# Kernel tuning notes

Measured on AMD Instinct MI355X. Metric: run time of the kernel, lower is better.

## Reference

```python
import jax, jax.numpy as jnp
import numpy as np

N = 50000      # nodes
E = 800000     # edges (avg degree 16)
F_IN = 128     # input_dim
HID = 64       # hidden_dim
HEADS = 4      # heads on first layer only
G = 512        # number of graphs in batch
EPS = 1e-5
NEG_SLOPE = 0.2

# (in_dim, out_dim, heads) per GATv2 layer
LAYER_DIMS = [(F_IN, HID, HEADS), (HID * HEADS, HID, 1), (HID, HID, 1)]


def setup_inputs() -> dict:
    key = jax.random.key(0)
    ks = jax.random.split(key, 16)
    def rn(k, shape, fan_in):
        return jax.random.normal(k, shape, jnp.float32) / np.float32(np.sqrt(fan_in))
    inp = {}
    inp["x"] = jax.random.normal(ks[0], (N, F_IN), jnp.float32)
    inp["edge_index"] = jax.random.randint(ks[1], (2, E), 0, N)
    inp["batch"] = jnp.sort(jax.random.randint(ks[2], (N,), 0, G))
    i = 3
    for l, (din, dout, h) in enumerate(LAYER_DIMS):
        kk = jax.random.split(ks[i], 3)
        inp[f"Wl{l}"] = rn(kk[0], (din, h * dout), din)
        inp[f"bl{l}"] = jnp.zeros((h * dout,), jnp.float32)
        inp[f"Wr{l}"] = rn(kk[1], (din, h * dout), din)
        inp[f"br{l}"] = jnp.zeros((h * dout,), jnp.float32)
        inp[f"att{l}"] = rn(kk[2], (h, dout), dout)
        inp[f"bias{l}"] = jnp.zeros((h * dout,), jnp.float32)
        inp[f"ln_g{l}"] = jnp.ones((h * dout,), jnp.float32)
        inp[f"ln_b{l}"] = jnp.zeros((h * dout,), jnp.float32)
        i += 1
    inp["Wh1"] = rn(ks[i], (HID, HID), HID)
    inp["bh1"] = jnp.zeros((HID,), jnp.float32)
    inp["Wh2"] = rn(ks[i + 1], (HID, 1), HID)
    inp["bh2"] = jnp.zeros((1,), jnp.float32)
    return inp


def gatv2_layer(x, src, dst, Wl, bl, Wr, br, att, bias, heads, out_c):
    """PyG GATv2Conv (concat=True, share_weights=False, eval mode)."""
    n = x.shape[0]
    xl = (x @ Wl + bl).reshape(n, heads, out_c)   # messages (source side)
    xr = (x @ Wr + br).reshape(n, heads, out_c)   # destination side
    e = jax.nn.leaky_relu(xl[src] + xr[dst], NEG_SLOPE)          # [E,H,C]
    logit = jnp.einsum('ehc,hc->eh', e, att)                      # [E,H]
    m = jax.ops.segment_max(logit, dst, num_segments=n)           # segment-softmax
    ex = jnp.exp(logit - m[dst])
    den = jax.ops.segment_sum(ex, dst, num_segments=n)
    alpha = ex / den[dst]                                         # [E,H]
    out = jax.ops.segment_sum(alpha[:, :, None] * xl[src], dst, num_segments=n)
    return out.reshape(n, heads * out_c) + bias


def graph_layernorm(h, g, b):
    """PyG LayerNorm(mode='graph') with batch=None: normalize over all elements."""
    mu = h.mean()
    xc = h - mu
    var = (xc * xc).mean()
    return xc * jax.lax.rsqrt(var + EPS) * g + b


def reference(x, edge_index, batch,
              Wl0, bl0, Wr0, br0, att0, bias0, ln_g0, ln_b0,
              Wl1, bl1, Wr1, br1, att1, bias1, ln_g1, ln_b1,
              Wl2, bl2, Wr2, br2, att2, bias2, ln_g2, ln_b2,
              Wh1, bh1, Wh2, bh2):
    src, dst = edge_index[0], edge_index[1]
    layers = [
        (Wl0, bl0, Wr0, br0, att0, bias0, ln_g0, ln_b0),
        (Wl1, bl1, Wr1, br1, att1, bias1, ln_g1, ln_b1),
        (Wl2, bl2, Wr2, br2, att2, bias2, ln_g2, ln_b2),
    ]
    h = x
    for (Wl, bl, Wr, br, att, bias, g, b), (_, dout, heads) in zip(layers, LAYER_DIMS):
        h_in = h
        h = gatv2_layer(h, src, dst, Wl, bl, Wr, br, att, bias, heads, dout)
        h = graph_layernorm(h, g, b)
        h = jax.nn.relu(h)
        if h_in.shape[1] == h.shape[1]:   # residual only when widths match
            h = h + h_in
        # dropout: identity in eval mode
    # global mean pool over graphs
    counts = jax.ops.segment_sum(jnp.ones((h.shape[0], 1), h.dtype), batch, num_segments=G)
    Z = jax.ops.segment_sum(h, batch, num_segments=G) / jnp.maximum(counts, 1.0)
    logits = jax.nn.relu(Z @ Wh1 + bh1) @ Wh2 + bh2
    return logits
```

## Files before the change

### kernel.cpp

```cpp
#include <hip/hip_runtime.h>
#include <math.h>

#define NN 50000
#define NE 800000
#define NG 512
#define LRELU 0.2f
#define LN_EPS 1e-5
#define GCAP 128
#define NBUCK 256

typedef __attribute__((ext_vector_type(8))) short short8;
typedef __attribute__((ext_vector_type(4))) float f32x4;

__global__ void hist_kernel(const int* __restrict__ dst, int* __restrict__ deg) {
    int e = blockIdx.x * blockDim.x + threadIdx.x;
    if (e < NE) atomicAdd(&deg[dst[e]], 1);
}

__global__ __launch_bounds__(1024) void scan1(const int* __restrict__ deg,
                                              int* __restrict__ excl,
                                              int* __restrict__ bsum, int n) {
    __shared__ int s[1024];
    int tid = threadIdx.x;
    int gid = blockIdx.x * 1024 + tid;
    int v = (gid < n) ? deg[gid] : 0;
    s[tid] = v;
    __syncthreads();
    for (int off = 1; off < 1024; off <<= 1) {
        int t = (tid >= off) ? s[tid - off] : 0;
        __syncthreads();
        s[tid] += t;
        __syncthreads();
    }
    if (gid < n) excl[gid] = s[tid] - v;
    if (tid == 1023) bsum[blockIdx.x] = s[1023];
}

__global__ __launch_bounds__(1024) void scan3(int* __restrict__ row_ptr,
                                              int* __restrict__ cursor,
                                              const int* __restrict__ bsum, int n) {
    __shared__ int sbase;
    int tid = threadIdx.x;
    if (tid < 64) {
        int v = (tid < (int)blockIdx.x) ? bsum[tid] : 0;
        #pragma unroll
        for (int off = 32; off > 0; off >>= 1) v += __shfl_xor(v, off, 64);
        if (tid == 0) sbase = v;
    }
    __syncthreads();
    int gid = blockIdx.x * 1024 + tid;
    if (gid < n) {
        int v = row_ptr[gid] + sbase;
        row_ptr[gid] = v;
        cursor[gid] = v;
    }
    if (gid == 0) row_ptr[n] = NE;
}

__global__ void scatter_kernel(const int* __restrict__ src, const int* __restrict__ dst,
                               int* __restrict__ cursor, int* __restrict__ col_src) {
    int e = blockIdx.x * blockDim.x + threadIdx.x;
    if (e < NE) {
        int pos = atomicAdd(&cursor[dst[e]], 1);
        col_src[pos] = src[e];
    }
}

__device__ inline void split_bf16(float v, ushort& h, ushort& l) {
    unsigned ub = __float_as_uint(v);
    unsigned hh = (ub + 0x7FFFu + ((ub >> 16) & 1u)) >> 16;
    float vh = __uint_as_float(hh << 16);
    float r = v - vh;
    unsigned ur = __float_as_uint(r);
    unsigned ll = (ur + 0x7FFFu + ((ur >> 16) & 1u)) >> 16;
    h = (ushort)hh; l = (ushort)ll;
}

__global__ __launch_bounds__(256) void prep_w(const float* __restrict__ Wl0,
                                              const float* __restrict__ Wr0,
                                              const float* __restrict__ Wl1,
                                              const float* __restrict__ Wr1,
                                              const float* __restrict__ Wl2,
                                              const float* __restrict__ Wr2,
                                              ushort* __restrict__ wt) {
    int id = blockIdx.x * 256 + threadIdx.x;
    const float* W; int K, N, rel; ushort* hi;
    if (id < 65536) {
        W = (id < 32768) ? Wl0 : Wr0;
        rel = id & 32767; K = 128; N = 256;
        hi = wt + ((id < 32768) ? 0 : 65536);
    } else if (id < 98304) {
        int t = id - 65536;
        W = (t < 16384) ? Wl1 : Wr1;
        rel = t & 16383; K = 256; N = 64;
        hi = wt + 131072 + ((t < 16384) ? 0 : 32768);
    } else if (id < 106496) {
        int t = id - 98304;
        W = (t < 4096) ? Wl2 : Wr2;
        rel = t & 4095; K = 64; N = 64;
        hi = wt + 196608 + ((t < 4096) ? 0 : 8192);
    } else return;
    ushort* lo = hi + K * N;
    int n = rel / K, k = rel - n * K;
    ushort h, l;
    split_bf16(W[k * N + n], h, l);
    hi[rel] = h;
    lo[rel] = l;
}

template<int NCB, bool DUAL, bool DOLN>
__global__ __launch_bounds__(256) void gemm_mfma(const float* __restrict__ A,
                                                 const ushort* __restrict__ Bh0,
                                                 const ushort* __restrict__ Bl0,
                                                 const float* __restrict__ bias0,
                                                 float* __restrict__ C0,
                                                 const ushort* __restrict__ Bh1,
                                                 const ushort* __restrict__ Bl1,
                                                 const float* __restrict__ bias1,
                                                 float* __restrict__ C1,
                                                 int M, int Ncol, int K,
                                                 const double* __restrict__ red,
                                                 int Mdiv,
                                                 const float* __restrict__ lng,
                                                 const float* __restrict__ lnb) {
    __shared__ ushort sAh[64][40];
    __shared__ ushort sAl[64][40];
    __shared__ ushort sBh[64 * NCB][40];
    __shared__ ushort sBl[64 * NCB][40];
    __shared__ float sstat[2];
    const ushort* Bhi = (!DUAL && blockIdx.y) ? Bh1 : Bh0;
    const ushort* Blo = (!DUAL && blockIdx.y) ? Bl1 : Bl0;
    const float*  biasS = (!DUAL && blockIdx.y) ? bias1 : bias0;
    float*        CS = (!DUAL && blockIdx.y) ? C1 : C0;
    const int tid = threadIdx.x;
    const int row0 = blockIdx.x * 64;
    const int w = tid >> 6, lane = tid & 63;
    const int fm = lane & 15;
    const int fk = (lane >> 4) * 8;
    float mu = 0.f, rstd = 0.f;
    if constexpr (DOLN) {
        if (tid < 64) {
            double sa = 0, sb = 0;
            for (int i = lane; i < NBUCK; i += 64) { sa += red[2 * i]; sb += red[2 * i + 1]; }
            #pragma unroll
            for (int off = 32; off > 0; off >>= 1) {
                sa += __shfl_xor(sa, off, 64);
                sb += __shfl_xor(sb, off, 64);
            }
            if (lane == 0) {
                double m_ = sa / Mdiv;
                double v_ = sb / Mdiv - m_ * m_;
                sstat[0] = (float)m_;
                sstat[1] = (float)(1.0 / sqrt(v_ + LN_EPS));
            }
        }
        __syncthreads();
        mu = sstat[0]; rstd = sstat[1];
    }
    f32x4 acc[4 * NCB] = {};

    for (int k0 = 0; k0 < K; k0 += 32) {
        __syncthreads();
        int f = tid;
        #pragma unroll
        for (int it = 0; it < 2; it++, f += 256) {
            int r = f >> 3, kc = (f & 7) * 4;
            int grow = row0 + r;
            float4 v = (grow < M) ? *(const float4*)&A[(size_t)grow * K + k0 + kc]
                                  : make_float4(0.f, 0.f, 0.f, 0.f);
            if constexpr (DOLN) {
                int c0 = k0 + kc;
                v.x = fmaxf((v.x - mu) * rstd * lng[c0 + 0] + lnb[c0 + 0], 0.f);
                v.y = fmaxf((v.y - mu) * rstd * lng[c0 + 1] + lnb[c0 + 1], 0.f);
                v.z = fmaxf((v.z - mu) * rstd * lng[c0 + 2] + lnb[c0 + 2], 0.f);
                v.w = fmaxf((v.w - mu) * rstd * lng[c0 + 3] + lnb[c0 + 3], 0.f);
            }
            ushort4 h, l;
            split_bf16(v.x, h.x, l.x);
            split_bf16(v.y, h.y, l.y);
            split_bf16(v.z, h.z, l.z);
            split_bf16(v.w, h.w, l.w);
            *(ushort4*)&sAh[r][kc] = h;
            *(ushort4*)&sAl[r][kc] = l;
        }
        int u = tid;
        #pragma unroll
        for (int it = 0; it < 2 * NCB; it++, u += 256) {
            int n = u >> 3, kc = (u & 7) * 4;
            const ushort* ph; const ushort* pl; int nr;
            if constexpr (DUAL) {
                bool s1 = n >= (32 * NCB);
                ph = s1 ? Bh1 : Bh0; pl = s1 ? Bl1 : Bl0;
                nr = s1 ? n - 32 * NCB : n;
            } else {
                ph = Bhi; pl = Blo; nr = n;
            }
            *(ushort4*)&sBh[n][kc] = *(const ushort4*)&ph[(size_t)nr * K + k0 + kc];
            *(ushort4*)&sBl[n][kc] = *(const ushort4*)&pl[(size_t)nr * K + k0 + kc];
        }
        __syncthreads();
        short8 ah = *(const short8*)&sAh[w * 16 + fm][fk];
        short8 al = *(const short8*)&sAl[w * 16 + fm][fk];
        #pragma unroll
        for (int c = 0; c < 4 * NCB; c++) {
            short8 bh = *(const short8*)&sBh[c * 16 + fm][fk];
            short8 bl = *(const short8*)&sBl[c * 16 + fm][fk];
            acc[c] = __builtin_amdgcn_mfma_f32_16x16x32_bf16(ah, bh, acc[c], 0, 0, 0);
            acc[c] = __builtin_amdgcn_mfma_f32_16x16x32_bf16(al, bh, acc[c], 0, 0, 0);
            acc[c] = __builtin_amdgcn_mfma_f32_16x16x32_bf16(ah, bl, acc[c], 0, 0, 0);
        }
    }
    const int orow = w * 16 + (lane >> 4) * 4;
    #pragma unroll
    for (int c = 0; c < 4 * NCB; c++) {
        float* Cp; const float* bp; int col;
        if constexpr (DUAL) {
            bool s1 = c >= 2 * NCB;
            Cp = s1 ? C1 : C0; bp = s1 ? bias1 : bias0;
            col = (s1 ? c - 2 * NCB : c) * 16 + fm;
        } else {
            Cp = CS; bp = biasS;
            col = c * 16 + fm;
        }
        float bv = bp[col];
        #pragma unroll
        for (int r = 0; r < 4; r++) {
            int grow = row0 + orow + r;
            if (grow < M) Cp[(size_t)grow * Ncol + col] = acc[c][r] + bv;
        }
    }
}

__device__ inline float dpp_red_add16(float x) {
    x += __int_as_float(__builtin_amdgcn_update_dpp(0, __float_as_int(x), 0xB1, 0xF, 0xF, true));
    x += __int_as_float(__builtin_amdgcn_update_dpp(0, __float_as_int(x), 0x4E, 0xF, 0xF, true));
    x += __int_as_float(__builtin_amdgcn_update_dpp(0, __float_as_int(x), 0x141, 0xF, 0xF, true));
    x += __int_as_float(__builtin_amdgcn_update_dpp(0, __float_as_int(x), 0x140, 0xF, 0xF, true));
    return x;
}

__device__ inline void gat_upd_fast(const float4& xv, const float4& rxr, const float4& ratt,
                                    float& m, float& sum, float4& acc) {
    float vx = xv.x + rxr.x; vx = fmaxf(vx, vx * LRELU);
    float vy = xv.y + rxr.y; vy = fmaxf(vy, vy * LRELU);
    float vz = xv.z + rxr.z; vz = fmaxf(vz, vz * LRELU);
    float vw = xv.w + rxr.w; vw = fmaxf(vw, vw * LRELU);
    float p = vx * ratt.x;
    p = fmaf(vy, ratt.y, p);
    p = fmaf(vz, ratt.z, p);
    p = fmaf(vw, ratt.w, p);
    p = dpp_red_add16(p);
    if (__all(p <= m)) {
        float e = __expf(p - m);
        sum += e;
        acc.x = fmaf(e, xv.x, acc.x);
        acc.y = fmaf(e, xv.y, acc.y);
        acc.z = fmaf(e, xv.z, acc.z);
        acc.w = fmaf(e, xv.w, acc.w);
    } else {
        float mn = fmaxf(m, p);
        float sc = __expf(m - mn);
        float e  = __expf(p - mn);
        sum = fmaf(sum, sc, e);
        acc.x = fmaf(acc.x, sc, e * xv.x);
        acc.y = fmaf(acc.y, sc, e * xv.y);
        acc.z = fmaf(acc.z, sc, e * xv.z);
        acc.w = fmaf(acc.w, sc, e * xv.w);
        m = mn;
    }
}

__global__ __launch_bounds__(256) void gat4(const float* __restrict__ xl,
                                            const float* __restrict__ xr,
                                            const float* __restrict__ att,
                                            const float* __restrict__ bias,
                                            const int* __restrict__ row_ptr,
                                            const int* __restrict__ col_src,
                                            float* __restrict__ out,
                                            double* __restrict__ red) {
    __shared__ int scol[4][GCAP];
    __shared__ double bs1[4], bs2[4];
    const int tid = threadIdx.x;
    const int w = tid >> 6, lane = tid & 63;
    const int n = blockIdx.x * 4 + w;
    const int base = row_ptr[n];
    int deg = row_ptr[n + 1] - base;
    if (deg > GCAP) deg = GCAP;
    for (int j = lane; j < deg; j += 64) scol[w][j] = col_src[base + j];
    const float4 rxr  = ((const float4*)(xr + (size_t)n * 256))[lane];
    const float4 ratt = ((const float4*)att)[lane];
    __syncthreads();

    float m = -1e30f, sum = 0.f;
    float4 acc = {0.f, 0.f, 0.f, 0.f};
    if (deg > 0) {
        const int dm1 = deg - 1;
        float4 xv0 = ((const float4*)(xl + (size_t)scol[w][0] * 256))[lane];
        float4 xv1 = ((const float4*)(xl + (size_t)scol[w][(1 < dm1) ? 1 : dm1] * 256))[lane];
        for (int j = 0; j < deg; j++) {
            float4 xv = xv0;
            xv0 = xv1;
            int idx = (j + 2 < deg) ? j + 2 : dm1;
            xv1 = ((const float4*)(xl + (size_t)scol[w][idx] * 256))[lane];
            gat_upd_fast(xv, rxr, ratt, m, sum, acc);
        }
    }
    float rden = (sum > 0.f) ? 1.f / sum : 0.f;
    float4 bv = ((const float4*)bias)[lane];
    float4 o;
    o.x = fmaf(acc.x, rden, bv.x);
    o.y = fmaf(acc.y, rden, bv.y);
    o.z = fmaf(acc.z, rden, bv.z);
    o.w = fmaf(acc.w, rden, bv.w);
    ((float4*)(out + (size_t)n * 256))[lane] = o;

    float z1 = o.x + o.y + o.z + o.w;
    float z2 = o.x * o.x + o.y * o.y + o.z * o.z + o.w * o.w;
    #pragma unroll
    for (int off = 32; off > 0; off >>= 1) {
        z1 += __shfl_xor(z1, off, 64);
        z2 += __shfl_xor(z2, off, 64);
    }
    if (lane == 0) { bs1[w] = (double)z1; bs2[w] = (double)z2; }
    __syncthreads();
    if (tid == 0) {
        double t1 = bs1[0] + bs1[1] + bs1[2] + bs1[3];
        double t2 = bs2[0] + bs2[1] + bs2[2] + bs2[3];
        int b = (blockIdx.x & (NBUCK - 1)) * 2;
        atomicAdd(&red[b], t1);
        atomicAdd(&red[b + 1], t2);
    }
}

__global__ __launch_bounds__(256) void gat1(const float* __restrict__ xl,
                                            const float* __restrict__ xr,
                                            const float* __restrict__ att,
                                            const float* __restrict__ bias,
                                            const int* __restrict__ row_ptr,
                                            const int* __restrict__ col_src,
                                            float* __restrict__ out,
                                            double* __restrict__ red) {
    __shared__ int scol[4][GCAP];
    __shared__ double bs1[4], bs2[4];
    const int tid = threadIdx.x;
    const int w = tid >> 6, lane = tid & 63;
    const int n = blockIdx.x * 4 + w;
    const int g = lane >> 4, li = lane & 15;
    const int base = row_ptr[n];
    int deg = row_ptr[n + 1] - base;
    if (deg > GCAP) deg = GCAP;
    for (int j = lane; j < deg; j += 64) scol[w][j] = col_src[base + j];
    const float4 rxr  = ((const float4*)(xr + (size_t)n * 64))[li];
    const float4 ratt = ((const float4*)att)[li];
    __syncthreads();

    float m = -1e30f, sum = 0.f;
    float4 acc = {0.f, 0.f, 0.f, 0.f};
    if (deg > 0) {
        const int dm1 = deg - 1;
        auto Lg = [&](int j) {
            int idx = (j < dm1) ? j : dm1;
            return ((const float4*)(xl + (size_t)scol[w][idx] * 64))[li];
        };
        float4 xv0 = Lg(g), xv1 = Lg(g + 4);
        for (int j = g; j < deg; j += 4) {
            float4 xv = xv0;
            xv0 = xv1;
            xv1 = Lg(j + 8);
            gat_upd_fast(xv, rxr, ratt, m, sum, acc);
        }
    }
    #pragma unroll
    for (int off = 16; off < 64; off <<= 1) {
        float m2 = __shfl_xor(m, off, 64);
        float z2 = __shfl_xor(sum, off, 64);
        float ax = __shfl_xor(acc.x, off, 64);
        float ay = __shfl_xor(acc.y, off, 64);
        float az = __shfl_xor(acc.z, off, 64);
        float aw = __shfl_xor(acc.w, off, 64);
        float M = fmaxf(m, m2);
        float e1 = __expf(m - M), e2 = __expf(m2 - M);
        sum   = sum   * e1 + z2 * e2;
        acc.x = acc.x * e1 + ax * e2;
        acc.y = acc.y * e1 + ay * e2;
        acc.z = acc.z * e1 + az * e2;
        acc.w = acc.w * e1 + aw * e2;
        m = M;
    }
    float rden = (sum > 0.f) ? 1.f / sum : 0.f;
    float4 bv = ((const float4*)bias)[li];
    float4 o;
    o.x = fmaf(acc.x, rden, bv.x);
    o.y = fmaf(acc.y, rden, bv.y);
    o.z = fmaf(acc.z, rden, bv.z);
    o.w = fmaf(acc.w, rden, bv.w);
    if (g == 0) ((float4*)(out + (size_t)n * 64))[li] = o;

    float z1 = (g == 0) ? (o.x + o.y + o.z + o.w) : 0.f;
    float z2 = (g == 0) ? (o.x * o.x + o.y * o.y + o.z * o.z + o.w * o.w) : 0.f;
    #pragma unroll
    for (int off = 32; off > 0; off >>= 1) {
        z1 += __shfl_xor(z1, off, 64);
        z2 += __shfl_xor(z2, off, 64);
    }
    if (lane == 0) { bs1[w] = (double)z1; bs2[w] = (double)z2; }
    __syncthreads();
    if (tid == 0) {
        double t1 = bs1[0] + bs1[1] + bs1[2] + bs1[3];
        double t2 = bs2[0] + bs2[1] + bs2[2] + bs2[3];
        int b = (blockIdx.x & (NBUCK - 1)) * 2;
        atomicAdd(&red[b], t1);
        atomicAdd(&red[b + 1], t2);
    }
}

#define PLB 256
__global__ __launch_bounds__(256) void pool_ln(const float* __restrict__ C2,
                                               const float* __restrict__ D,
                                               const double* __restrict__ red,
                                               const float* __restrict__ g1,
                                               const float* __restrict__ b1,
                                               const float* __restrict__ g2,
                                               const float* __restrict__ b2,
                                               const int* __restrict__ batch,
                                               float* __restrict__ Zsum,
                                               int* __restrict__ gcount) {
    __shared__ float sst[4];
    const int w = threadIdx.x >> 6;
    const int lane = threadIdx.x & 63;
    if (w < 2) {
        const double* rp = red + (w + 1) * 2 * NBUCK;
        double sa = 0, sb = 0;
        for (int i = lane; i < NBUCK; i += 64) { sa += rp[2 * i]; sb += rp[2 * i + 1]; }
        #pragma unroll
        for (int off = 32; off > 0; off >>= 1) {
            sa += __shfl_xor(sa, off, 64);
            sb += __shfl_xor(sb, off, 64);
        }
        if (lane == 0) {
            double m_ = sa / (double)(NN * 64);
            double v_ = sb / (double)(NN * 64) - m_ * m_;
            sst[w * 2]     = (float)m_;
            sst[w * 2 + 1] = (float)(1.0 / sqrt(v_ + LN_EPS));
        }
    }
    __syncthreads();
    const float mu1 = sst[0], r1 = sst[1], mu2 = sst[2], r2 = sst[3];
    const int wid = blockIdx.x * 4 + w;
    const int NW = PLB * 4;
    const int per = (NN + NW - 1) / NW;
    int n0 = wid * per;
    int n1 = n0 + per; if (n1 > NN) n1 = NN;
    if (n0 >= n1) return;
    const float ga = r1 * g1[lane], ba = fmaf(-mu1, ga, b1[lane]);
    const float gb = r2 * g2[lane], bb = fmaf(-mu2, gb, b2[lane]);
    float zacc = 0.f; int cnt = 0; int cur = batch[n0];
    for (int n = n0; n < n1; n++) {
        int gi = batch[n];
        if (gi != cur) {
            atomicAdd(&Zsum[cur * 64 + lane], zacc);
            if (lane == 0) atomicAdd(&gcount[cur], cnt);
            zacc = 0.f; cnt = 0; cur = gi;
        }
        float hin = fmaxf(fmaf(D[(size_t)n * 64 + lane], ga, ba), 0.f);
        float v = fmaxf(fmaf(C2[(size_t)n * 64 + lane], gb, bb), 0.f) + hin;
        zacc += v; cnt++;
    }
    atomicAdd(&Zsum[cur * 64 + lane], zacc);
    if (lane == 0) atomicAdd(&gcount[cur], cnt);
}

__global__ __launch_bounds__(64) void mlp_head(const float* __restrict__ Zsum,
                                               const int* __restrict__ gcount,
                                               const float* __restrict__ Wh1,
                                               const float* __restrict__ bh1,
                                               const float* __restrict__ Wh2,
                                               const float* __restrict__ bh2,
                                               float* __restrict__ out) {
    __shared__ float sz[64];
    int g = blockIdx.x, tid = threadIdx.x;
    int cnt = gcount[g];
    float inv = 1.f / (float)(cnt > 1 ? cnt : 1);
    sz[tid] = Zsum[g * 64 + tid] * inv;
    __syncthreads();
    float acc = bh1[tid];
    #pragma unroll
    for (int c = 0; c < 64; c++) acc = fmaf(sz[c], Wh1[c * 64 + tid], acc);
    acc = fmaxf(acc, 0.f);
    float v = acc * Wh2[tid];
    #pragma unroll
    for (int off = 32; off > 0; off >>= 1) v += __shfl_xor(v, off, 64);
    if (tid == 0) out[g] = v + bh2[0];
}

extern "C" void kernel_launch(void* const* d_in, const int* in_sizes, int n_in,
                              void* d_out, int out_size, void* d_ws, size_t ws_size,
                              hipStream_t stream) {
    (void)in_sizes; (void)n_in; (void)out_size; (void)ws_size;
    const float* x     = (const float*)d_in[0];
    const int*   ei    = (const int*)d_in[1];
    const int*   batch = (const int*)d_in[2];
    const float* Wl0 = (const float*)d_in[3];  const float* bl0 = (const float*)d_in[4];
    const float* Wr0 = (const float*)d_in[5];  const float* br0 = (const float*)d_in[6];
    const float* at0 = (const float*)d_in[7];  const float* bi0 = (const float*)d_in[8];
    const float* lg0 = (const float*)d_in[9];  const float* lb0 = (const float*)d_in[10];
    const float* Wl1 = (const float*)d_in[11]; const float* bl1 = (const float*)d_in[12];
    const float* Wr1 = (const float*)d_in[13]; const float* br1 = (const float*)d_in[14];
    const float* at1 = (const float*)d_in[15]; const float* bi1 = (const float*)d_in[16];
    const float* lg1 = (const float*)d_in[17]; const float* lb1 = (const float*)d_in[18];
    const float* Wl2 = (const float*)d_in[19]; const float* bl2 = (const float*)d_in[20];
    const float* Wr2 = (const float*)d_in[21]; const float* br2 = (const float*)d_in[22];
    const float* at2 = (const float*)d_in[23]; const float* bi2 = (const float*)d_in[24];
    const float* lg2 = (const float*)d_in[25]; const float* lb2 = (const float*)d_in[26];
    const float* Wh1 = (const float*)d_in[27]; const float* bh1 = (const float*)d_in[28];
    const float* Wh2 = (const float*)d_in[29]; const float* bh2 = (const float*)d_in[30];
    float* out = (float*)d_out;

    const int* srcp = ei;
    const int* dstp = ei + NE;

    char* w = (char*)d_ws;
    size_t off = 0;
    auto carve = [&](size_t bytes) -> void* {
        void* p = w + off;
        off += (bytes + 255) & ~(size_t)255;
        return p;
    };
    float* A = (float*)carve((size_t)NN * 256 * 4);
    float* B = (float*)carve((size_t)NN * 256 * 4);
    float* C = (float*)carve((size_t)NN * 256 * 4);
    float* D = (float*)carve((size_t)NN * 64 * 4);
    ushort* wt = (ushort*)carve(212992 * 2);
    const size_t REDB = (size_t)3 * NBUCK * 2 * sizeof(double);
    size_t zbytes = REDB + (size_t)NG * 64 * 4 + NG * 4 + (size_t)NN * 4;
    char* zb = (char*)carve(zbytes);
    double* red   = (double*)zb;
    float*  Zsum  = (float*)(zb + REDB);
    int*    gcnt  = (int*)(zb + REDB + (size_t)NG * 64 * 4);
    int*    deg   = (int*)(zb + REDB + (size_t)NG * 64 * 4 + NG * 4);
    int* row_ptr = (int*)carve((size_t)(NN + 1) * 4);
    int* cursor  = (int*)carve((size_t)NN * 4);
    int* col_src = (int*)carve((size_t)NE * 4);
    int* bsum    = (int*)carve(64 * 4);

    const ushort* W0lh = wt;           const ushort* W0ll = wt + 32768;
    const ushort* W0rh = wt + 65536;   const ushort* W0rl = wt + 98304;
    const ushort* W1lh = wt + 131072;  const ushort* W1ll = wt + 147456;
    const ushort* W1rh = wt + 163840;  const ushort* W1rl = wt + 180224;
    const ushort* W2lh = wt + 196608;  const ushort* W2ll = wt + 200704;
    const ushort* W2rh = wt + 204800;  const ushort* W2rl = wt + 208896;

    hipMemsetAsync(zb, 0, zbytes, stream);
    prep_w<<<416, 256, 0, stream>>>(Wl0, Wr0, Wl1, Wr1, Wl2, Wr2, wt);

    hist_kernel<<<(NE + 255) / 256, 256, 0, stream>>>(dstp, deg);
    const int SB = (NN + 1023) / 1024;
    scan1<<<SB, 1024, 0, stream>>>(deg, row_ptr, bsum, NN);
    scan3<<<SB, 1024, 0, stream>>>(row_ptr, cursor, bsum, NN);
    scatter_kernel<<<(NE + 255) / 256, 256, 0, stream>>>(srcp, dstp, cursor, col_src);

    const int GR = (NN + 63) / 64;
    const int GATB = NN / 4;

    gemm_mfma<4, false, false><<<dim3(GR, 2), 256, 0, stream>>>(
        x, W0lh, W0ll, bl0, A, W0rh, W0rl, br0, B, NN, 256, 128,
        nullptr, 1, nullptr, nullptr);
    gat4<<<GATB, 256, 0, stream>>>(A, B, at0, bi0, row_ptr, col_src, C, red);

    gemm_mfma<2, true, true><<<dim3(GR), 256, 0, stream>>>(
        C, W1lh, W1ll, bl1, A, W1rh, W1rl, br1, B, NN, 64, 256,
        red, NN * 256, lg0, lb0);
    gat1<<<GATB, 256, 0, stream>>>(A, B, at1, bi1, row_ptr, col_src, D, red + 2 * NBUCK);

    gemm_mfma<2, true, true><<<dim3(GR), 256, 0, stream>>>(
        D, W2lh, W2ll, bl2, A, W2rh, W2rl, br2, B, NN, 64, 64,
        red + 2 * NBUCK, NN * 64, lg1, lb1);
    gat1<<<GATB, 256, 0, stream>>>(A, B, at2, bi2, row_ptr, col_src, C, red + 4 * NBUCK);

    pool_ln<<<PLB, 256, 0, stream>>>(C, D, red, lg1, lb1, lg2, lb2,
                                     batch, Zsum, gcnt);
    mlp_head<<<NG, 64, 0, stream>>>(Zsum, gcnt, Wh1, bh1, Wh2, bh2, out);
}
```

Measured before the change: 549.1 us.

## Fuse CSR build kernels with weight prep and first GEMM; split GAT4 online softmax

Merges the degree histogram into the weight-prep launch and the CSR scatter into the layer-0 GEMM launch, so the independent work shares a launch and can overlap. The scatter blocks use a grid-stride loop over 1024 blocks. In the 4-head GAT kernel, the neighbour loop now keeps two independent online-softmax accumulators processed in pairs and merges them at the end, which shortens the dependency chain. The price is more registers and a different reduction order in floating point.

```diff
diff --git a/kernel.cpp b/kernel.cpp
--- a/kernel.cpp
+++ b/kernel.cpp
@@ -8,14 +8,11 @@
 #define LN_EPS 1e-5
 #define GCAP 128
 #define NBUCK 256
+#define GRB 782
+#define SCB 1024
 
 typedef __attribute__((ext_vector_type(8))) short short8;
 typedef __attribute__((ext_vector_type(4))) float f32x4;
-
-__global__ void hist_kernel(const int* __restrict__ dst, int* __restrict__ deg) {
-    int e = blockIdx.x * blockDim.x + threadIdx.x;
-    if (e < NE) atomicAdd(&deg[dst[e]], 1);
-}
 
 __global__ __launch_bounds__(1024) void scan1(const int* __restrict__ deg,
                                               int* __restrict__ excl,
@@ -57,15 +54,6 @@
     if (gid == 0) row_ptr[n] = NE;
 }
 
-__global__ void scatter_kernel(const int* __restrict__ src, const int* __restrict__ dst,
-                               int* __restrict__ cursor, int* __restrict__ col_src) {
-    int e = blockIdx.x * blockDim.x + threadIdx.x;
-    if (e < NE) {
-        int pos = atomicAdd(&cursor[dst[e]], 1);
-        col_src[pos] = src[e];
-    }
-}
-
 __device__ inline void split_bf16(float v, ushort& h, ushort& l) {
     unsigned ub = __float_as_uint(v);
     unsigned hh = (ub + 0x7FFFu + ((ub >> 16) & 1u)) >> 16;
@@ -76,14 +64,22 @@
     h = (ushort)hh; l = (ushort)ll;
 }
 
-__global__ __launch_bounds__(256) void prep_w(const float* __restrict__ Wl0,
-                                              const float* __restrict__ Wr0,
-                                              const float* __restrict__ Wl1,
-                                              const float* __restrict__ Wr1,
-                                              const float* __restrict__ Wl2,
-                                              const float* __restrict__ Wr2,
-                                              ushort* __restrict__ wt) {
-    int id = blockIdx.x * 256 + threadIdx.x;
+__global__ __launch_bounds__(256) void prep_hist(const float* __restrict__ Wl0,
+                                                 const float* __restrict__ Wr0,
+                                                 const float* __restrict__ Wl1,
+                                                 const float* __restrict__ Wr1,
+                                                 const float* __restrict__ Wl2,
+                                                 const float* __restrict__ Wr2,
+                                                 ushort* __restrict__ wt,
+                                                 const int* __restrict__ dst,
+                                                 int* __restrict__ deg) {
+    int bid = blockIdx.x;
+    if (bid >= 416) {
+        int e = (bid - 416) * 256 + threadIdx.x;
+        if (e < NE) atomicAdd(&deg[dst[e]], 1);
+        return;
+    }
+    int id = bid * 256 + threadIdx.x;
     const float* W; int K, N, rel; ushort* hi;
     if (id < 65536) {
         W = (id < 32768) ? Wl0 : Wr0;
@@ -109,31 +105,32 @@
 }
 
 template<int NCB, bool DUAL, bool DOLN>
-__global__ __launch_bounds__(256) void gemm_mfma(const float* __restrict__ A,
-                                                 const ushort* __restrict__ Bh0,
-                                                 const ushort* __restrict__ Bl0,
-                                                 const float* __restrict__ bias0,
-                                                 float* __restrict__ C0,
-                                                 const ushort* __restrict__ Bh1,
-                                                 const ushort* __restrict__ Bl1,
-                                                 const float* __restrict__ bias1,
-                                                 float* __restrict__ C1,
-                                                 int M, int Ncol, int K,
-                                                 const double* __restrict__ red,
-                                                 int Mdiv,
-                                                 const float* __restrict__ lng,
-                                                 const float* __restrict__ lnb) {
+__device__ __forceinline__ void gemm_body(const float* __restrict__ A,
+                                          const ushort* __restrict__ Bh0,
+                                          const ushort* __restrict__ Bl0,
+                                          const float* __restrict__ bias0,
+                                          float* __restrict__ C0,
+                                          const ushort* __restrict__ Bh1,
+                                          const ushort* __restrict__ Bl1,
+                                          const float* __restrict__ bias1,
+                                          float* __restrict__ C1,
+                                          int M, int Ncol, int K,
+                                          const double* __restrict__ red,
+                                          int Mdiv,
+                                          const float* __restrict__ lng,
+                                          const float* __restrict__ lnb,
+                                          int bx, int by) {
     __shared__ ushort sAh[64][40];
     __shared__ ushort sAl[64][40];
     __shared__ ushort sBh[64 * NCB][40];
     __shared__ ushort sBl[64 * NCB][40];
     __shared__ float sstat[2];
-    const ushort* Bhi = (!DUAL && blockIdx.y) ? Bh1 : Bh0;
-    const ushort* Blo = (!DUAL && blockIdx.y) ? Bl1 : Bl0;
-    const float*  biasS = (!DUAL && blockIdx.y) ? bias1 : bias0;
-    float*        CS = (!DUAL && blockIdx.y) ? C1 : C0;
+    const ushort* Bhi = (!DUAL && by) ? Bh1 : Bh0;
+    const ushort* Blo = (!DUAL && by) ? Bl1 : Bl0;
+    const float*  biasS = (!DUAL && by) ? bias1 : bias0;
+    float*        CS = (!DUAL && by) ? C1 : C0;
     const int tid = threadIdx.x;
-    const int row0 = blockIdx.x * 64;
+    const int row0 = bx * 64;
     const int w = tid >> 6, lane = tid & 63;
     const int fm = lane & 15;
     const int fk = (lane >> 4) * 8;
@@ -228,6 +225,53 @@
             int grow = row0 + orow + r;
             if (grow < M) Cp[(size_t)grow * Ncol + col] = acc[c][r] + bv;
         }
+    }
+}
+
+template<int NCB, bool DUAL, bool DOLN>
+__global__ __launch_bounds__(256) void gemm_mfma(const float* __restrict__ A,
+                                                 const ushort* __restrict__ Bh0,
+                                                 const ushort* __restrict__ Bl0,
+                                                 const float* __restrict__ bias0,
+                                                 float* __restrict__ C0,
+                                                 const ushort* __restrict__ Bh1,
+                                                 const ushort* __restrict__ Bl1,
+                                                 const float* __restrict__ bias1,
+                                                 float* __restrict__ C1,
+                                                 int M, int Ncol, int K,
+                                                 const double* __restrict__ red,
+                                                 int Mdiv,
+                                                 const float* __restrict__ lng,
+                                                 const float* __restrict__ lnb) {
+    gemm_body<NCB, DUAL, DOLN>(A, Bh0, Bl0, bias0, C0, Bh1, Bl1, bias1, C1,
+                               M, Ncol, K, red, Mdiv, lng, lnb,
+                               blockIdx.x, blockIdx.y);
+}
+
+__global__ __launch_bounds__(256) void gemm0_scatter(const float* __restrict__ A,
+                                                     const ushort* __restrict__ Bh0,
+                                                     const ushort* __restrict__ Bl0,
+                                                     const float* __restrict__ bias0,
+                                                     float* __restrict__ C0,
+                                                     const ushort* __restrict__ Bh1,
+                                                     const ushort* __restrict__ Bl1,
+                                                     const float* __restrict__ bias1,
+                                                     float* __restrict__ C1,
+                                                     const int* __restrict__ src,
+                                                     const int* __restrict__ dst,
+                                                     int* __restrict__ cursor,
+                                                     int* __restrict__ col_src) {
+    int bid = blockIdx.x;
+    if (bid < 2 * GRB) {
+        gemm_body<4, false, false>(A, Bh0, Bl0, bias0, C0, Bh1, Bl1, bias1, C1,
+                                   NN, 256, 128, nullptr, 1, nullptr, nullptr,
+                                   bid % GRB, bid / GRB);
+        return;
+    }
+    int b = bid - 2 * GRB;
+    for (int e = b * 256 + threadIdx.x; e < NE; e += SCB * 256) {
+        int pos = atomicAdd(&cursor[dst[e]], 1);
+        col_src[pos] = src[e];
     }
 }
 
@@ -291,20 +335,33 @@
     const float4 ratt = ((const float4*)att)[lane];
     __syncthreads();
 
-    float m = -1e30f, sum = 0.f;
-    float4 acc = {0.f, 0.f, 0.f, 0.f};
+    float m0 = -1e30f, s0 = 0.f, m1 = -1e30f, s1 = 0.f;
+    float4 a0 = {0.f, 0.f, 0.f, 0.f}, a1 = {0.f, 0.f, 0.f, 0.f};
     if (deg > 0) {
         const int dm1 = deg - 1;
-        float4 xv0 = ((const float4*)(xl + (size_t)scol[w][0] * 256))[lane];
-        float4 xv1 = ((const float4*)(xl + (size_t)scol[w][(1 < dm1) ? 1 : dm1] * 256))[lane];
-        for (int j = 0; j < deg; j++) {
-            float4 xv = xv0;
-            xv0 = xv1;
-            int idx = (j + 2 < deg) ? j + 2 : dm1;
-            xv1 = ((const float4*)(xl + (size_t)scol[w][idx] * 256))[lane];
-            gat_upd_fast(xv, rxr, ratt, m, sum, acc);
-        }
-    }
+        auto LD = [&](int j) {
+            int idx = (j < dm1) ? j : dm1;
+            return ((const float4*)(xl + (size_t)scol[w][idx] * 256))[lane];
+        };
+        float4 b0 = LD(0), b1 = LD(1);
+        int j = 0;
+        for (; j + 2 <= deg; j += 2) {
+            float4 x0 = b0, x1 = b1;
+            b0 = LD(j + 2); b1 = LD(j + 3);
+            gat_upd_fast(x0, rxr, ratt, m0, s0, a0);
+            gat_upd_fast(x1, rxr, ratt, m1, s1, a1);
+        }
+        if (j < deg) gat_upd_fast(b0, rxr, ratt, m0, s0, a0);
+    }
+    float M = fmaxf(m0, m1);
+    float e0 = __expf(m0 - M), e1 = __expf(m1 - M);
+    float sum = s0 * e0 + s1 * e1;
+    float4 acc;
+    acc.x = a0.x * e0 + a1.x * e1;
+    acc.y = a0.y * e0 + a1.y * e1;
+    acc.z = a0.z * e0 + a1.z * e1;
+    acc.w = a0.w * e0 + a1.w * e1;
+
     float rden = (sum > 0.f) ? 1.f / sum : 0.f;
     float4 bv = ((const float4*)bias)[lane];
     float4 o;
@@ -551,28 +608,26 @@
     const ushort* W2rh = wt + 204800;  const ushort* W2rl = wt + 208896;
 
     hipMemsetAsync(zb, 0, zbytes, stream);
-    prep_w<<<416, 256, 0, stream>>>(Wl0, Wr0, Wl1, Wr1, Wl2, Wr2, wt);
-
-    hist_kernel<<<(NE + 255) / 256, 256, 0, stream>>>(dstp, deg);
+
+    prep_hist<<<416 + (NE + 255) / 256, 256, 0, stream>>>(Wl0, Wr0, Wl1, Wr1, Wl2, Wr2,
+                                                          wt, dstp, deg);
     const int SB = (NN + 1023) / 1024;
     scan1<<<SB, 1024, 0, stream>>>(deg, row_ptr, bsum, NN);
     scan3<<<SB, 1024, 0, stream>>>(row_ptr, cursor, bsum, NN);
-    scatter_kernel<<<(NE + 255) / 256, 256, 0, stream>>>(srcp, dstp, cursor, col_src);
-
-    const int GR = (NN + 63) / 64;
+
     const int GATB = NN / 4;
 
-    gemm_mfma<4, false, false><<<dim3(GR, 2), 256, 0, stream>>>(
-        x, W0lh, W0ll, bl0, A, W0rh, W0rl, br0, B, NN, 256, 128,
-        nullptr, 1, nullptr, nullptr);
+    gemm0_scatter<<<2 * GRB + SCB, 256, 0, stream>>>(
+        x, W0lh, W0ll, bl0, A, W0rh, W0rl, br0, B,
+        srcp, dstp, cursor, col_src);
     gat4<<<GATB, 256, 0, stream>>>(A, B, at0, bi0, row_ptr, col_src, C, red);
 
-    gemm_mfma<2, true, true><<<dim3(GR), 256, 0, stream>>>(
+    gemm_mfma<2, true, true><<<dim3(GRB), 256, 0, stream>>>(
         C, W1lh, W1ll, bl1, A, W1rh, W1rl, br1, B, NN, 64, 256,
         red, NN * 256, lg0, lb0);
     gat1<<<GATB, 256, 0, stream>>>(A, B, at1, bi1, row_ptr, col_src, D, red + 2 * NBUCK);
 
-    gemm_mfma<2, true, true><<<dim3(GR), 256, 0, stream>>>(
+    gemm_mfma<2, true, true><<<dim3(GRB), 256, 0, stream>>>(
         D, W2lh, W2ll, bl2, A, W2rh, W2rl, br2, B, NN, 64, 64,
         red + 2 * NBUCK, NN * 64, lg1, lb1);
     gat1<<<GATB, 256, 0, stream>>>(A, B, at2, bi2, row_ptr, col_src, C, red + 4 * NBUCK);
```

After: 555.5 us. No clear change (+1.2%).
